# Performance work log

Measured on AMD Instinct MI355X. Metric: run time of the kernel, lower is better.

The kernel has to match this reference:

```python
import jax, jax.numpy as jnp
import numpy as np

N = 16384
DIMS = [3, 256, 256, 256, 256, 256, 256, 3]
NU = 1.0 / 100.0  # 1 / Reynold


def setup_inputs() -> dict:
    key = jax.random.key(0)
    ks = jax.random.split(key, 3 + 2 * (len(DIMS) - 1))
    inp = {
        "t": jax.random.uniform(ks[0], (N, 1), dtype=jnp.float32),
        "x": jax.random.uniform(ks[1], (N, 1), dtype=jnp.float32),
        "y": jax.random.uniform(ks[2], (N, 1), dtype=jnp.float32),
    }
    for i in range(len(DIMS) - 1):
        fan_in, fan_out = DIMS[i], DIMS[i + 1]
        # glorot_normal scale
        scale = jnp.sqrt(2.0 / (fan_in + fan_out)).astype(jnp.float32)
        inp[f"W{i}"] = jax.random.normal(ks[3 + 2 * i], (fan_in, fan_out), dtype=jnp.float32) * scale
        inp[f"b{i}"] = jax.random.normal(ks[4 + 2 * i], (fan_out,), dtype=jnp.float32) * 0.01
    return inp


def _mlp(p, params):
    # p: [3] single (t,x,y) point -> [3] (u,v,p)
    h = p
    for W, b in params[:-1]:
        h = jnp.sin(h @ W + b)
    W, b = params[-1]
    return h @ W + b


def reference(t, x, y, W0, b0, W1, b1, W2, b2, W3, b3, W4, b4, W5, b5, W6, b6):
    params = [(W0, b0), (W1, b1), (W2, b2), (W3, b3), (W4, b4), (W5, b5), (W6, b6)]
    f = lambda p: _mlp(p, params)
    txy = jnp.concatenate([t, x, y], axis=1)  # [N, 3]

    uvp = jax.vmap(f)(txy)                          # [N, 3]
    J = jax.vmap(jax.jacfwd(f))(txy)                # [N, 3(out), 3(in)]
    H = jax.vmap(jax.jacfwd(jax.jacfwd(f)))(txy)    # [N, 3(out), 3(in), 3(in)]

    u, v = uvp[:, 0], uvp[:, 1]
    u_t, u_x, u_y = J[:, 0, 0], J[:, 0, 1], J[:, 0, 2]
    v_t, v_x, v_y = J[:, 1, 0], J[:, 1, 1], J[:, 1, 2]
    p_x, p_y = J[:, 2, 1], J[:, 2, 2]
    u_xx, u_yy = H[:, 0, 1, 1], H[:, 0, 2, 2]
    v_xx, v_yy = H[:, 1, 1, 1], H[:, 1, 2, 2]

    eq1 = u_t + (u * u_x + v * u_y) + p_x - NU * (u_xx + u_yy)
    eq2 = v_t + (u * v_x + v * v_y) + p_y - NU * (v_xx + v_yy)
    eq3 = u_x + v_y
    return eq1[:, None], eq2[:, None], eq3[:, None]
```

## Files before the change

kernel.cpp:

```cpp
#include <hip/hip_runtime.h>

#define NPTS 16384
#define PW 16
#define NU (1.0f / 100.0f)

typedef _Float16 f16;
typedef __attribute__((ext_vector_type(4))) _Float16 f16x4;
typedef __attribute__((ext_vector_type(8))) _Float16 f16x8;
typedef __attribute__((ext_vector_type(4))) float f32x4;

__device__ __forceinline__ int swz(int g) { return g ^ ((g >> 3) & 7); }

__global__ __launch_bounds__(256) void prep_kernel(
    const float* __restrict__ W1, const float* __restrict__ W2,
    const float* __restrict__ W3, const float* __restrict__ W4,
    const float* __restrict__ W5, const float* __restrict__ W6,
    f16* __restrict__ bh, f16* __restrict__ b6h)
{
    int idx = blockIdx.x * 256 + threadIdx.x;
    if (idx < 40960) {
        int col = idx & 255, subk = (idx >> 8) & 3, kc = (idx >> 10) & 7, L = idx >> 13;
        const float* W = (L == 0) ? W1 : (L == 1) ? W2 : (L == 2) ? W3 : (L == 3) ? W4 : W5;
        f16x8 vh;
        #pragma unroll
        for (int j = 0; j < 8; ++j) {
            int k = kc * 32 + subk * 8 + j;
            vh[j] = (f16)W[k * 256 + col];
        }
        int nf = col >> 4, l15 = col & 15, lane = subk * 16 + l15;
        *(f16x8*)(bh + (((L * 8 + kc) * 16 + nf) * 64 + lane) * 8) = vh;
    } else {
        int u = idx - 40960;
        if (u < 512) {
            int col = u & 15, subk = (u >> 4) & 3, kc = u >> 6;
            f16x8 vh;
            #pragma unroll
            for (int j = 0; j < 8; ++j) {
                int k = kc * 32 + subk * 8 + j;
                vh[j] = (f16)((col < 3) ? W6[k * 3 + col] : 0.f);
            }
            *(f16x8*)(b6h + (kc * 64 + subk * 16 + col) * 8) = vh;
        }
    }
}

__global__ __launch_bounds__(256) void pinn_ns_mfma(
    const float* __restrict__ t_, const float* __restrict__ x_, const float* __restrict__ y_,
    const float* __restrict__ W0, const float* __restrict__ b0,
    const float* __restrict__ b1, const float* __restrict__ b2,
    const float* __restrict__ b3, const float* __restrict__ b4,
    const float* __restrict__ b5, const float* __restrict__ b6,
    const f16* __restrict__ bh, const f16* __restrict__ b6h,
    float* __restrict__ out)
{
    __shared__ __align__(16) f16 afrag[6 * 8 * 512];

    const int tid = threadIdx.x;
    const int lane = tid & 63;
    const int nq = tid >> 6;
    const int q = lane >> 4;
    const int s = lane & 15;
    const int gl = swz(lane);
    const int p0 = blockIdx.x * PW;

    {
        float tv = t_[p0 + s], xv = x_[p0 + s], yv = y_[p0 + s];
        int fq0 = tid >> 4;
        #pragma unroll
        for (int i = 0; i < 4; ++i) {
            int fq = fq0 + 16 * i;
            int f0 = fq * 4;
            f32x4 w0 = *(const f32x4*)&W0[f0];
            f32x4 w1 = *(const f32x4*)&W0[256 + f0];
            f32x4 w2 = *(const f32x4*)&W0[512 + f0];
            f32x4 bb = *(const f32x4*)&b0[f0];
            f16x4 o[6];
            #pragma unroll
            for (int ff = 0; ff < 4; ++ff) {
                float z = tv * w0[ff] + xv * w1[ff] + yv * w2[ff] + bb[ff];
                float sv, cv;
                __sincosf(z, &sv, &cv);
                o[0][ff] = (f16)sv;
                o[1][ff] = (f16)(cv * w0[ff]);
                o[2][ff] = (f16)(cv * w1[ff]);
                o[3][ff] = (f16)(cv * w2[ff]);
                o[4][ff] = (f16)(-sv * w1[ff] * w1[ff]);
                o[5][ff] = (f16)(-sv * w2[ff] * w2[ff]);
            }
            int kc = fq >> 3;
            int g = swz(16 * ((fq >> 1) & 3) + s);
            int half = fq & 1;
            #pragma unroll
            for (int c = 0; c < 6; ++c)
                *(f16x4*)&afrag[(c * 8 + kc) * 512 + g * 8 + half * 4] = o[c];
        }
    }
    __syncthreads();

    const float* bias[5] = {b1, b2, b3, b4, b5};
    const f16x8* A = (const f16x8*)afrag;
    for (int L = 0; L < 5; ++L) {
        const f16x8* wH = (const f16x8*)bh + L * 8192;
        f32x4 acc[6][4];
        #pragma unroll
        for (int c = 0; c < 6; ++c)
            #pragma unroll
            for (int f = 0; f < 4; ++f)
                acc[c][f] = (f32x4){0.f, 0.f, 0.f, 0.f};

        f16x8 Wc[4];
        #pragma unroll
        for (int f = 0; f < 4; ++f)
            Wc[f] = wH[(nq * 4 + f) * 64 + lane];

        #pragma unroll
        for (int kc = 0; kc < 8; ++kc) {
            f16x8 Wn[4];
            if (kc < 7) {
                #pragma unroll
                for (int f = 0; f < 4; ++f)
                    Wn[f] = wH[((kc + 1) * 16 + nq * 4 + f) * 64 + lane];
            }
            f16x8 S[6];
            #pragma unroll
            for (int c = 0; c < 6; ++c)
                S[c] = A[(c * 8 + kc) * 64 + gl];
            #pragma unroll
            for (int c = 0; c < 6; ++c)
                #pragma unroll
                for (int f = 0; f < 4; ++f)
                    acc[c][f] = __builtin_amdgcn_mfma_f32_16x16x32_f16(Wc[f], S[c], acc[c][f], 0, 0, 0);
            if (kc < 7) {
                #pragma unroll
                for (int f = 0; f < 4; ++f)
                    Wc[f] = Wn[f];
            }
        }
        __syncthreads();

        const float* bbp = bias[L];
        #pragma unroll
        for (int mf = 0; mf < 4; ++mf) {
            int fbase = nq * 64 + mf * 16 + 4 * q;
            f32x4 bq = *(const f32x4*)&bbp[fbase];
            f16x4 o[6];
            #pragma unroll
            for (int r = 0; r < 4; ++r) {
                float z = acc[0][mf][r] + bq[r];
                float zt = acc[1][mf][r], zx = acc[2][mf][r], zy = acc[3][mf][r];
                float zxx = acc[4][mf][r], zyy = acc[5][mf][r];
                float sv, cv;
                __sincosf(z, &sv, &cv);
                o[0][r] = (f16)sv;
                o[1][r] = (f16)(cv * zt);
                o[2][r] = (f16)(cv * zx);
                o[3][r] = (f16)(cv * zy);
                o[4][r] = (f16)(cv * zxx - sv * zx * zx);
                o[5][r] = (f16)(cv * zyy - sv * zy * zy);
            }
            int kc = 2 * nq + (mf >> 1);
            int g = swz(16 * (2 * (mf & 1) + (q >> 1)) + s);
            int half = q & 1;
            #pragma unroll
            for (int c = 0; c < 6; ++c)
                *(f16x4*)&afrag[(c * 8 + kc) * 512 + g * 8 + half * 4] = o[c];
        }
        __syncthreads();
    }

    if (nq == 0) {
        f32x4 a6[6];
        #pragma unroll
        for (int c = 0; c < 6; ++c)
            a6[c] = (f32x4){0.f, 0.f, 0.f, 0.f};
        const f16x8* w6 = (const f16x8*)b6h;
        #pragma unroll
        for (int kc = 0; kc < 8; ++kc) {
            f16x8 Wf = w6[kc * 64 + lane];
            #pragma unroll
            for (int c = 0; c < 6; ++c)
                a6[c] = __builtin_amdgcn_mfma_f32_16x16x32_f16(Wf, A[(c * 8 + kc) * 64 + gl], a6[c], 0, 0, 0);
        }
        if (lane < 16) {
            int g = p0 + s;
            float u_  = a6[0][0] + b6[0], v_ = a6[0][1] + b6[1];
            float ut  = a6[1][0], vt  = a6[1][1];
            float ux  = a6[2][0], vx  = a6[2][1], px = a6[2][2];
            float uy  = a6[3][0], vy  = a6[3][1], py = a6[3][2];
            float uxx = a6[4][0], vxx = a6[4][1];
            float uyy = a6[5][0], vyy = a6[5][1];
            out[g]            = ut + (u_ * ux + v_ * uy) + px - NU * (uxx + uyy);
            out[NPTS + g]     = vt + (u_ * vx + v_ * vy) + py - NU * (vxx + vyy);
            out[2 * NPTS + g] = ux + vy;
        }
    }
}

extern "C" void kernel_launch(void* const* d_in, const int* in_sizes, int n_in,
                              void* d_out, int out_size, void* d_ws, size_t ws_size,
                              hipStream_t stream) {
    const float* t_ = (const float*)d_in[0];
    const float* x_ = (const float*)d_in[1];
    const float* y_ = (const float*)d_in[2];
    const float* W[7];
    const float* b[7];
    for (int i = 0; i < 7; ++i) {
        W[i] = (const float*)d_in[3 + 2 * i];
        b[i] = (const float*)d_in[4 + 2 * i];
    }
    float* out = (float*)d_out;

    f16* bh  = (f16*)d_ws;
    f16* b6h = bh + 5 * 65536;

    hipLaunchKernelGGL(prep_kernel, dim3(162), dim3(256), 0, stream,
                       W[1], W[2], W[3], W[4], W[5], W[6], bh, b6h);
    hipLaunchKernelGGL(pinn_ns_mfma, dim3(NPTS / PW), dim3(256), 0, stream,
                       t_, x_, y_, W[0], b[0],
                       b[1], b[2], b[3], b[4], b[5], b[6],
                       bh, b6h, out);
}
```

Baseline: 146.6 us.

## Propagate Laplacian as one channel instead of separate xx and yy channels

Forward-mode propagation now merges the second-derivative channels for x and y into one Laplacian channel. This works because the operator is linear and only u_xx+u_yy is needed. Channels drop from six to five, which removes about a sixth of the MFMA work, LDS traffic and accumulator registers in every hidden layer. Rounding changes slightly, since the two second-derivative terms are summed before the f16 conversion.

```diff
diff --git a/kernel.cpp b/kernel.cpp
--- a/kernel.cpp
+++ b/kernel.cpp
@@ -2,6 +2,7 @@
 
 #define NPTS 16384
 #define PW 16
+#define NCH 5
 #define NU (1.0f / 100.0f)
 
 typedef _Float16 f16;
@@ -53,7 +54,7 @@
     const f16* __restrict__ bh, const f16* __restrict__ b6h,
     float* __restrict__ out)
 {
-    __shared__ __align__(16) f16 afrag[6 * 8 * 512];
+    __shared__ __align__(16) f16 afrag[NCH * 8 * 512];
 
     const int tid = threadIdx.x;
     const int lane = tid & 63;
@@ -74,7 +75,7 @@
             f32x4 w1 = *(const f32x4*)&W0[256 + f0];
             f32x4 w2 = *(const f32x4*)&W0[512 + f0];
             f32x4 bb = *(const f32x4*)&b0[f0];
-            f16x4 o[6];
+            f16x4 o[NCH];
             #pragma unroll
             for (int ff = 0; ff < 4; ++ff) {
                 float z = tv * w0[ff] + xv * w1[ff] + yv * w2[ff] + bb[ff];
@@ -84,14 +85,13 @@
                 o[1][ff] = (f16)(cv * w0[ff]);
                 o[2][ff] = (f16)(cv * w1[ff]);
                 o[3][ff] = (f16)(cv * w2[ff]);
-                o[4][ff] = (f16)(-sv * w1[ff] * w1[ff]);
-                o[5][ff] = (f16)(-sv * w2[ff] * w2[ff]);
+                o[4][ff] = (f16)(-sv * (w1[ff] * w1[ff] + w2[ff] * w2[ff]));
             }
             int kc = fq >> 3;
             int g = swz(16 * ((fq >> 1) & 3) + s);
             int half = fq & 1;
             #pragma unroll
-            for (int c = 0; c < 6; ++c)
+            for (int c = 0; c < NCH; ++c)
                 *(f16x4*)&afrag[(c * 8 + kc) * 512 + g * 8 + half * 4] = o[c];
         }
     }
@@ -101,9 +101,9 @@
     const f16x8* A = (const f16x8*)afrag;
     for (int L = 0; L < 5; ++L) {
         const f16x8* wH = (const f16x8*)bh + L * 8192;
-        f32x4 acc[6][4];
-        #pragma unroll
-        for (int c = 0; c < 6; ++c)
+        f32x4 acc[NCH][4];
+        #pragma unroll
+        for (int c = 0; c < NCH; ++c)
             #pragma unroll
             for (int f = 0; f < 4; ++f)
                 acc[c][f] = (f32x4){0.f, 0.f, 0.f, 0.f};
@@ -121,12 +121,12 @@
                 for (int f = 0; f < 4; ++f)
                     Wn[f] = wH[((kc + 1) * 16 + nq * 4 + f) * 64 + lane];
             }
-            f16x8 S[6];
-            #pragma unroll
-            for (int c = 0; c < 6; ++c)
+            f16x8 S[NCH];
+            #pragma unroll
+            for (int c = 0; c < NCH; ++c)
                 S[c] = A[(c * 8 + kc) * 64 + gl];
             #pragma unroll
-            for (int c = 0; c < 6; ++c)
+            for (int c = 0; c < NCH; ++c)
                 #pragma unroll
                 for (int f = 0; f < 4; ++f)
                     acc[c][f] = __builtin_amdgcn_mfma_f32_16x16x32_f16(Wc[f], S[c], acc[c][f], 0, 0, 0);
@@ -143,54 +143,52 @@
         for (int mf = 0; mf < 4; ++mf) {
             int fbase = nq * 64 + mf * 16 + 4 * q;
             f32x4 bq = *(const f32x4*)&bbp[fbase];
-            f16x4 o[6];
+            f16x4 o[NCH];
             #pragma unroll
             for (int r = 0; r < 4; ++r) {
                 float z = acc[0][mf][r] + bq[r];
                 float zt = acc[1][mf][r], zx = acc[2][mf][r], zy = acc[3][mf][r];
-                float zxx = acc[4][mf][r], zyy = acc[5][mf][r];
+                float zlap = acc[4][mf][r];
                 float sv, cv;
                 __sincosf(z, &sv, &cv);
                 o[0][r] = (f16)sv;
                 o[1][r] = (f16)(cv * zt);
                 o[2][r] = (f16)(cv * zx);
                 o[3][r] = (f16)(cv * zy);
-                o[4][r] = (f16)(cv * zxx - sv * zx * zx);
-                o[5][r] = (f16)(cv * zyy - sv * zy * zy);
+                o[4][r] = (f16)(cv * zlap - sv * (zx * zx + zy * zy));
             }
             int kc = 2 * nq + (mf >> 1);
             int g = swz(16 * (2 * (mf & 1) + (q >> 1)) + s);
             int half = q & 1;
             #pragma unroll
-            for (int c = 0; c < 6; ++c)
+            for (int c = 0; c < NCH; ++c)
                 *(f16x4*)&afrag[(c * 8 + kc) * 512 + g * 8 + half * 4] = o[c];
         }
         __syncthreads();
     }
 
     if (nq == 0) {
-        f32x4 a6[6];
-        #pragma unroll
-        for (int c = 0; c < 6; ++c)
+        f32x4 a6[NCH];
+        #pragma unroll
+        for (int c = 0; c < NCH; ++c)
             a6[c] = (f32x4){0.f, 0.f, 0.f, 0.f};
         const f16x8* w6 = (const f16x8*)b6h;
         #pragma unroll
         for (int kc = 0; kc < 8; ++kc) {
             f16x8 Wf = w6[kc * 64 + lane];
             #pragma unroll
-            for (int c = 0; c < 6; ++c)
+            for (int c = 0; c < NCH; ++c)
                 a6[c] = __builtin_amdgcn_mfma_f32_16x16x32_f16(Wf, A[(c * 8 + kc) * 64 + gl], a6[c], 0, 0, 0);
         }
         if (lane < 16) {
             int g = p0 + s;
-            float u_  = a6[0][0] + b6[0], v_ = a6[0][1] + b6[1];
-            float ut  = a6[1][0], vt  = a6[1][1];
-            float ux  = a6[2][0], vx  = a6[2][1], px = a6[2][2];
-            float uy  = a6[3][0], vy  = a6[3][1], py = a6[3][2];
-            float uxx = a6[4][0], vxx = a6[4][1];
-            float uyy = a6[5][0], vyy = a6[5][1];
-            out[g]            = ut + (u_ * ux + v_ * uy) + px - NU * (uxx + uyy);
-            out[NPTS + g]     = vt + (u_ * vx + v_ * vy) + py - NU * (vxx + vyy);
+            float u_   = a6[0][0] + b6[0], v_ = a6[0][1] + b6[1];
+            float ut   = a6[1][0], vt   = a6[1][1];
+            float ux   = a6[2][0], vx   = a6[2][1], px = a6[2][2];
+            float uy   = a6[3][0], vy   = a6[3][1], py = a6[3][2];
+            float ulap = a6[4][0], vlap = a6[4][1];
+            out[g]            = ut + (u_ * ux + v_ * uy) + px - NU * ulap;
+            out[NPTS + g]     = vt + (u_ * vx + v_ * vy) + py - NU * vlap;
             out[2 * NPTS + g] = ux + vy;
         }
     }
```

Result: no change. 143.8 us (-1.9%).
